# Kernel optimization log

Measured on AMD Instinct MI355X. Metric: run time of the kernel, lower is better.

Reference implementation:

```python
import jax, jax.numpy as jnp
import numpy as np

N = 16384          # total samples (row 0 = anchor)
NPOS = N // 2      # labels: first half == 1 (positives), second half == 0 (negatives)
NNEG = N - NPOS
D = 128            # embedding dim
ALPHA = 0.5
MARGIN = 1.0
TEMPERATURE = 1.0
EPS = 1e-8
SQRT2 = 1.4142135623730951


def setup_inputs() -> dict:
    key = jax.random.key(0)
    k1, k2 = jax.random.split(key)
    est_means = jax.random.normal(k1, (N, D), dtype=jnp.float32)
    # variances must be positive
    est_vars = jax.random.uniform(k2, (N, D), dtype=jnp.float32, minval=0.01, maxval=1.0)
    # deterministic half/half labels so n_pos, n_neg are static (JIT-friendly)
    y_true = jnp.concatenate([jnp.ones((NPOS,), jnp.int32), jnp.zeros((NNEG,), jnp.int32)])
    return {"y_true": y_true, "est_means": est_means, "est_vars": est_vars, "NmulPnN": float(N)}


def reference(y_true, est_means, est_vars, NmulPnN):
    # static-size nonzero (exact counts by construction)
    idx_pos = jnp.nonzero(y_true == 1, size=NPOS)[0]
    idx_neg = jnp.nonzero(y_true == 0, size=NNEG)[0]

    muA = est_means[0]          # [D]
    varA = est_vars[0]          # [D]
    muP = est_means[idx_pos]    # [P, D]
    varP = est_vars[idx_pos]
    muN = est_means[idx_neg]    # [Q, D]
    varN = est_vars[idx_neg]

    muA2 = muA * muA
    muP2 = muP * muP
    muN2 = muN * muN

    # mu[i,j] = sum_d (muP2+varP-2 muA muP)[i,d] - sum_d (muN2+varN-2 muA muN)[j,d]
    sP = jnp.sum(muP2 + varP - 2.0 * muA * muP, axis=1)   # [P]
    sN = jnp.sum(muN2 + varN - 2.0 * muA * muN, axis=1)   # [Q]
    mu = sP[:, None] - sN[None, :]                        # [P, Q]

    # variance terms: T1 depends only on P, T2 only on N, T3 = 4 muP muN varA (cross)
    T1 = (varP * varP + 2.0 * muP2 * varP + 2.0 * (varA + muA2) * (varP + muP2)
          - 2.0 * muA2 * muP2 - 4.0 * muA * muP * varP)
    T2 = (varN * varN + 2.0 * muN2 * varN + 2.0 * (varA + muA2) * (varN + muN2)
          - 2.0 * muA2 * muN2 - 4.0 * muA * muN * varN)
    t1 = jnp.sum(T1, axis=1)                              # [P]
    t2 = jnp.sum(T2, axis=1)                              # [Q]
    cross = jnp.einsum('pd,qd->pq', muP * varA, muN)      # sum_d muP muN varA -> [P, Q]

    sigma2 = 2.0 * t1[:, None] + 2.0 * t2[None, :] - 8.0 * cross
    sigma = jnp.sqrt(jnp.clip(sigma2, 0.0))

    # Normal(mu, sigma+eps).cdf(margin/temperature)
    x = (MARGIN / TEMPERATURE - mu) / (sigma + EPS)
    probs = 0.5 * (1.0 + jax.lax.erf(x / SQRT2))

    loss = -jnp.sum(jnp.log(probs + EPS))
    const_ = NmulPnN / (ALPHA * float(NPOS * NNEG))
    return const_ * loss
```

## Files before the change

kernel.cpp:

```cpp
#include <hip/hip_runtime.h>
#include <hip/hip_bf16.h>

#define NTOT 16384
#define NP   8192
#define NQ   8192
#define DIM  128

typedef float f32x4 __attribute__((ext_vector_type(4)));
typedef __bf16 bf16x8 __attribute__((ext_vector_type(8)));

__device__ __forceinline__ float wave_reduce_sum(float v) {
#pragma unroll
    for (int off = 32; off > 0; off >>= 1)
        v += __shfl_xor(v, off, 64);
    return v;
}

__global__ __launch_bounds__(256)
void ptl_prep(const float* __restrict__ means,
              const float* __restrict__ vars,
              __hip_bfloat16* __restrict__ pv,
              __hip_bfloat16* __restrict__ nb,
              float2* __restrict__ rowPack,
              float2* __restrict__ colPack)
{
    const int wid  = threadIdx.x >> 6;
    const int lane = threadIdx.x & 63;
    const int r    = (blockIdx.x << 2) + wid;
    const int d    = lane << 1;

    const float2 mu   = *reinterpret_cast<const float2*>(means + (size_t)r * DIM + d);
    const float2 var  = *reinterpret_cast<const float2*>(vars  + (size_t)r * DIM + d);
    const float2 muA  = *reinterpret_cast<const float2*>(means + d);
    const float2 varA = *reinterpret_cast<const float2*>(vars  + d);

    float s = 0.f, t = 0.f;
    {
        const float m = mu.x, v = var.x, ma = muA.x, va = varA.x;
        const float m2 = m * m, ma2 = ma * ma;
        s += m2 + v - 2.f * ma * m;
        t += v * v + 2.f * m2 * v + 2.f * (va + ma2) * (v + m2)
           - 2.f * ma2 * m2 - 4.f * ma * m * v;
    }
    {
        const float m = mu.y, v = var.y, ma = muA.y, va = varA.y;
        const float m2 = m * m, ma2 = ma * ma;
        s += m2 + v - 2.f * ma * m;
        t += v * v + 2.f * m2 * v + 2.f * (va + ma2) * (v + m2)
           - 2.f * ma2 * m2 - 4.f * ma * m * v;
    }
    s = wave_reduce_sum(s);
    t = wave_reduce_sum(t);

    if (r < NP) {
        __hip_bfloat162 pb;
        pb.x = __float2bfloat16(mu.x * varA.x);
        pb.y = __float2bfloat16(mu.y * varA.y);
        *reinterpret_cast<__hip_bfloat162*>(pv + (size_t)r * DIM + d) = pb;
        if (lane == 0) rowPack[r] = make_float2(1.f - s, 2.f * t);
    } else {
        const int q = r - NP;
        __hip_bfloat162 qb;
        qb.x = __float2bfloat16(mu.x);
        qb.y = __float2bfloat16(mu.y);
        *reinterpret_cast<__hip_bfloat162*>(nb + (size_t)q * DIM + d) = qb;
        if (lane == 0) colPack[q] = make_float2(s, 2.f * t);
    }
}

__global__ __launch_bounds__(256)
void ptl_main(const __hip_bfloat16* __restrict__ pv,
              const __hip_bfloat16* __restrict__ nb,
              const float2* __restrict__ rowPack,
              const float2* __restrict__ colPack,
              const float* __restrict__ nmul,
              float* __restrict__ out)
{
    const int wid  = threadIdx.x >> 6;
    const int lane = threadIdx.x & 63;
    const int bi   = blockIdx.x >> 6;
    const int bj   = blockIdx.x & 63;
    const int wr   = wid >> 1, wc = wid & 1;
    const int i0   = bi * 128 + wr * 64;
    const int j0   = bj * 128 + wc * 64;
    const int l16  = lane & 15;
    const int l4   = lane >> 4;

    f32x4 acc[4][4];
#pragma unroll
    for (int m = 0; m < 4; ++m)
#pragma unroll
        for (int n = 0; n < 4; ++n)
            acc[m][n] = (f32x4){0.f, 0.f, 0.f, 0.f};

    const __hip_bfloat16* Ab = pv + (size_t)(i0 + l16) * DIM + l4 * 8;
    const __hip_bfloat16* Bb = nb + (size_t)(j0 + l16) * DIM + l4 * 8;

#pragma unroll
    for (int kq = 0; kq < 4; ++kq) {
        bf16x8 a[4], b[4];
#pragma unroll
        for (int m = 0; m < 4; ++m)
            a[m] = *reinterpret_cast<const bf16x8*>(Ab + m * 16 * DIM + kq * 32);
#pragma unroll
        for (int n = 0; n < 4; ++n)
            b[n] = *reinterpret_cast<const bf16x8*>(Bb + n * 16 * DIM + kq * 32);
#pragma unroll
        for (int m = 0; m < 4; ++m)
#pragma unroll
            for (int n = 0; n < 4; ++n)
                acc[m][n] = __builtin_amdgcn_mfma_f32_16x16x32_bf16(a[m], b[n], acc[m][n], 0, 0, 0);
    }

    float2 cp[4];
#pragma unroll
    for (int n = 0; n < 4; ++n)
        cp[n] = colPack[j0 + n * 16 + l16];

    float lacc0 = 0.f, lacc1 = 0.f, lacc2 = 0.f, lacc3 = 0.f;
#pragma unroll
    for (int m = 0; m < 4; ++m) {
        float2 rp[4];
#pragma unroll
        for (int rr = 0; rr < 4; ++rr)
            rp[rr] = rowPack[i0 + m * 16 + l4 * 4 + rr];
#pragma unroll
        for (int n = 0; n < 4; ++n) {
#pragma unroll
            for (int rr = 0; rr < 4; ++rr) {
                const float c   = acc[m][n][rr];
                const float t12 = rp[rr].y + cp[n].y;
                const float omm = rp[rr].x + cp[n].x;
                float s2 = fmaf(-8.f, c, t12);
                s2 = fmaxf(s2, 1e-16f);
                const float inv_sigma = __builtin_amdgcn_rsqf(s2);
                const float z  = omm * inv_sigma * 0.7071067811865475f;
                const float az = fabsf(z);
                const float tt = __builtin_amdgcn_rcpf(fmaf(0.3275911f, az, 1.f));
                float poly = fmaf(tt, 1.061405429f, -1.453152027f);
                poly = fmaf(tt, poly, 1.421413741f);
                poly = fmaf(tt, poly, -0.284496736f);
                poly = fmaf(tt, poly, 0.254829592f);
                poly *= tt;
                const float e = __expf(-az * az);
                const float erfc_ = poly * e;
                const float probs = (z >= 0.f) ? fmaf(-0.5f, erfc_, 1.f) : 0.5f * erfc_;
                const float lg = __logf(probs + 1e-8f);
                if (rr == 0) lacc0 += lg;
                else if (rr == 1) lacc1 += lg;
                else if (rr == 2) lacc2 += lg;
                else lacc3 += lg;
            }
        }
    }

    float lsum = (lacc0 + lacc1) + (lacc2 + lacc3);
    lsum = wave_reduce_sum(lsum);

    __shared__ float wsum[4];
    if (lane == 0) wsum[wid] = lsum;
    __syncthreads();
    if (threadIdx.x == 0) {
        const float bsum = (wsum[0] + wsum[1]) + (wsum[2] + wsum[3]);
        const float cst = nmul[0] / (0.5f * (float)NP * (float)NQ);
        atomicAdd(out, -cst * bsum);
    }
}

extern "C" void kernel_launch(void* const* d_in, const int* in_sizes, int n_in,
                              void* d_out, int out_size, void* d_ws, size_t ws_size,
                              hipStream_t stream)
{
    const float* means = (const float*)d_in[1];
    const float* vars  = (const float*)d_in[2];
    const float* nmul  = (const float*)d_in[3];
    float* out = (float*)d_out;

    __hip_bfloat16* pv = (__hip_bfloat16*)d_ws;
    __hip_bfloat16* nb = pv + (size_t)NP * DIM;
    float2* rowPack = (float2*)((char*)d_ws + (size_t)(NP + NQ) * DIM * sizeof(__hip_bfloat16));
    float2* colPack = rowPack + NP;

    hipMemsetAsync(d_out, 0, sizeof(float), stream);
    ptl_prep<<<NTOT / 4, 256, 0, stream>>>(means, vars, pv, nb, rowPack, colPack);
    ptl_main<<<(NP / 128) * (NQ / 128), 256, 0, stream>>>(pv, nb, rowPack, colPack, nmul, out);
}
```

Before: 161.5 us.

## Replace erf/log epilogue with LDS lookup table of -log(Phi) with linear interpolation

Precomputes a table of -log(0.5*erfc(-x/sqrt2)+eps) over x in [-8,8) with step 1/128, packed as a bf16 value and bf16 slope, in the prep kernel. The main kernel copies it into shared memory twice (one copy per lane parity, to spread bank conflicts) and replaces the per-element rsq/rcp/polynomial/exp/log chain with one table read and an fma. This cuts transcendental and VALU work in the elementwise epilogue, at the cost of bf16 table precision, clamping of arguments outside [-8,8), an extra LDS fill plus barrier per block, and possible LDS bank conflicts on the gathers.

```diff
diff --git a/kernel.cpp b/kernel.cpp
--- a/kernel.cpp
+++ b/kernel.cpp
@@ -1,10 +1,14 @@
 #include <hip/hip_runtime.h>
 #include <hip/hip_bf16.h>
+#include <math.h>
 
 #define NTOT 16384
 #define NP   8192
 #define NQ   8192
 #define DIM  128
+#define TBLN 2048
+#define TBL_SCALE 128.0f
+#define INV_SQRT2 0.70710678118654752f
 
 typedef float f32x4 __attribute__((ext_vector_type(4)));
 typedef __bf16 bf16x8 __attribute__((ext_vector_type(8)));
@@ -14,6 +18,12 @@
     for (int off = 32; off > 0; off >>= 1)
         v += __shfl_xor(v, off, 64);
     return v;
+}
+
+__device__ __forceinline__ unsigned short f32_to_bf16_rne(float f) {
+    unsigned u = __float_as_uint(f);
+    u += 0x7FFFu + ((u >> 16) & 1u);
+    return (unsigned short)(u >> 16);
 }
 
 __global__ __launch_bounds__(256)
@@ -22,7 +32,8 @@
               __hip_bfloat16* __restrict__ pv,
               __hip_bfloat16* __restrict__ nb,
               float2* __restrict__ rowPack,
-              float2* __restrict__ colPack)
+              float2* __restrict__ colPack,
+              unsigned* __restrict__ tblG)
 {
     const int wid  = threadIdx.x >> 6;
     const int lane = threadIdx.x & 63;
@@ -66,6 +77,17 @@
         *reinterpret_cast<__hip_bfloat162*>(nb + (size_t)q * DIM + d) = qb;
         if (lane == 0) colPack[q] = make_float2(s, 2.f * t);
     }
+
+    if (blockIdx.x < 8) {
+        const int k = blockIdx.x * 256 + threadIdx.x;
+        const float x0 = -8.f + (float)k / TBL_SCALE;
+        const float x1 = -8.f + (float)(k + 1) / TBL_SCALE;
+        const float g0 = -logf(0.5f * erfcf(-x0 * INV_SQRT2) + 1e-8f);
+        const float g1 = -logf(0.5f * erfcf(-x1 * INV_SQRT2) + 1e-8f);
+        const unsigned short gb = f32_to_bf16_rne(g0);
+        const unsigned short db = f32_to_bf16_rne(g1 - g0);
+        tblG[k] = ((unsigned)db << 16) | (unsigned)gb;
+    }
 }
 
 __global__ __launch_bounds__(256)
@@ -73,6 +95,7 @@
               const __hip_bfloat16* __restrict__ nb,
               const float2* __restrict__ rowPack,
               const float2* __restrict__ colPack,
+              const unsigned* __restrict__ tblG,
               const float* __restrict__ nmul,
               float* __restrict__ out)
 {
@@ -86,6 +109,19 @@
     const int l16  = lane & 15;
     const int l4   = lane >> 4;
 
+    __shared__ unsigned tbl[2 * TBLN];
+    {
+        const uint4* gt4 = (const uint4*)tblG;
+        uint4* lt4 = (uint4*)tbl;
+#pragma unroll
+        for (int t = threadIdx.x; t < TBLN / 4; t += 256) {
+            const uint4 v = gt4[t];
+            lt4[t] = v;
+            lt4[t + TBLN / 4] = v;
+        }
+    }
+    __syncthreads();
+
     f32x4 acc[4][4];
 #pragma unroll
     for (int m = 0; m < 4; ++m)
@@ -116,6 +152,8 @@
 #pragma unroll
     for (int n = 0; n < 4; ++n)
         cp[n] = colPack[j0 + n * 16 + l16];
+
+    const unsigned laneSel = ((unsigned)lane & 1u) << 11;
 
     float lacc0 = 0.f, lacc1 = 0.f, lacc2 = 0.f, lacc3 = 0.f;
 #pragma unroll
@@ -132,24 +170,20 @@
                 const float t12 = rp[rr].y + cp[n].y;
                 const float omm = rp[rr].x + cp[n].x;
                 float s2 = fmaf(-8.f, c, t12);
-                s2 = fmaxf(s2, 1e-16f);
-                const float inv_sigma = __builtin_amdgcn_rsqf(s2);
-                const float z  = omm * inv_sigma * 0.7071067811865475f;
-                const float az = fabsf(z);
-                const float tt = __builtin_amdgcn_rcpf(fmaf(0.3275911f, az, 1.f));
-                float poly = fmaf(tt, 1.061405429f, -1.453152027f);
-                poly = fmaf(tt, poly, 1.421413741f);
-                poly = fmaf(tt, poly, -0.284496736f);
-                poly = fmaf(tt, poly, 0.254829592f);
-                poly *= tt;
-                const float e = __expf(-az * az);
-                const float erfc_ = poly * e;
-                const float probs = (z >= 0.f) ? fmaf(-0.5f, erfc_, 1.f) : 0.5f * erfc_;
-                const float lg = __logf(probs + 1e-8f);
-                if (rr == 0) lacc0 += lg;
-                else if (rr == 1) lacc1 += lg;
-                else if (rr == 2) lacc2 += lg;
-                else lacc3 += lg;
+                s2 = fmaxf(s2, 1e-20f);
+                const float x = omm * __builtin_amdgcn_rsqf(s2);
+                float u = fmaf(x, TBL_SCALE, 1024.0f);
+                u = __builtin_amdgcn_fmed3f(u, 0.0f, 2047.999f);
+                const unsigned iu = (unsigned)u;
+                const float fr = u - (float)iu;
+                const unsigned pk = tbl[iu + laneSel];
+                const float g  = __uint_as_float(pk << 16);
+                const float dg = __uint_as_float(pk & 0xFFFF0000u);
+                const float val = fmaf(fr, dg, g);
+                if (rr == 0) lacc0 += val;
+                else if (rr == 1) lacc1 += val;
+                else if (rr == 2) lacc2 += val;
+                else lacc3 += val;
             }
         }
     }
@@ -163,7 +197,7 @@
     if (threadIdx.x == 0) {
         const float bsum = (wsum[0] + wsum[1]) + (wsum[2] + wsum[3]);
         const float cst = nmul[0] / (0.5f * (float)NP * (float)NQ);
-        atomicAdd(out, -cst * bsum);
+        atomicAdd(out, cst * bsum);
     }
 }
 
@@ -180,8 +214,9 @@
     __hip_bfloat16* nb = pv + (size_t)NP * DIM;
     float2* rowPack = (float2*)((char*)d_ws + (size_t)(NP + NQ) * DIM * sizeof(__hip_bfloat16));
     float2* colPack = rowPack + NP;
+    unsigned* tblG  = (unsigned*)(colPack + NQ);
 
     hipMemsetAsync(d_out, 0, sizeof(float), stream);
-    ptl_prep<<<NTOT / 4, 256, 0, stream>>>(means, vars, pv, nb, rowPack, colPack);
-    ptl_main<<<(NP / 128) * (NQ / 128), 256, 0, stream>>>(pv, nb, rowPack, colPack, nmul, out);
-}
+    ptl_prep<<<NTOT / 4, 256, 0, stream>>>(means, vars, pv, nb, rowPack, colPack, tblG);
+    ptl_main<<<(NP / 128) * (NQ / 128), 256, 0, stream>>>(pv, nb, rowPack, colPack, tblG, nmul, out);
+}
```

After: 159.1 us. No clear change (-1.4%).
